# Optimization experiments

Hardware: AMD Instinct MI355X
Metric: run time of the kernel (lower is better)

## Reference

```python
import jax, jax.numpy as jnp
import numpy as np

BNK, L, DIN, DOUT, NREL = 1280, 64, 512, 256, 40

def setup_inputs() -> dict:
    key = jax.random.key(0)
    ks = jax.random.split(key, 10)
    rep = jax.random.normal(ks[0], (BNK, L, DIN), dtype=jnp.float32)
    # adj_arc_in[..., 0] = flattened sentence index, adj_arc_in[..., 1] = head token position
    sent = jnp.broadcast_to(jnp.arange(BNK, dtype=jnp.int64)[:, None], (BNK, L))
    head = jax.random.randint(ks[1], (BNK, L), 0, L, dtype=jnp.int64)
    adj_arc_in = jnp.stack([sent, head], axis=-1)  # [BNK, L, 2]
    adj_lab_in = jax.random.randint(ks[2], (BNK, L), 0, NREL, dtype=jnp.int64)
    adj_mask_in = (jax.random.uniform(ks[3], (BNK, L)) < 0.9).astype(jnp.float32)
    adj_mask_loop = jnp.ones((BNK, L), dtype=jnp.float32)
    mask = jnp.ones((BNK, L), dtype=jnp.float32)
    # parameters (xavier-ish init)
    W_in = jax.random.normal(ks[4], (DIN, DOUT), dtype=jnp.float32) * (2.0 / (DIN + DOUT)) ** 0.5
    b_in = jnp.zeros((NREL, DOUT), dtype=jnp.float32)
    W_gate_in = jax.random.uniform(ks[5], (DIN, 1), dtype=jnp.float32)
    b_gate_in = jnp.ones((NREL, 1), dtype=jnp.float32)
    W_self = jax.random.normal(ks[6], (DIN, DOUT), dtype=jnp.float32) * (2.0 / (DIN + DOUT)) ** 0.5
    W_gate_self = jax.random.uniform(ks[7], (DIN, 1), dtype=jnp.float32)
    return {"rep": rep, "adj_mask_in": adj_mask_in, "adj_mask_loop": adj_mask_loop,
            "mask": mask, "W_in": W_in, "b_in": b_in, "W_gate_in": W_gate_in,
            "b_gate_in": b_gate_in, "W_self": W_self, "W_gate_self": W_gate_self,
            "adj_arc_in": adj_arc_in, "adj_lab_in": adj_lab_in}

def reference(rep, adj_mask_in, adj_mask_loop, mask, W_in, b_in, W_gate_in,
              b_gate_in, W_self, W_gate_self, adj_arc_in, adj_lab_in):
    bnk, l, din = rep.shape
    dout = W_in.shape[1]
    rep_ = rep.reshape(bnk * l, din)                    # [M, Din]
    idx = adj_arc_in[..., 0].reshape(-1) * l + adj_arc_in[..., 1].reshape(-1)  # [M]
    lab = adj_lab_in.reshape(-1)                        # [M]
    # in-arc potential: gather projected head token, add relation-typed bias
    in_pot = (rep_ @ W_in)[idx] + b_in[lab]             # [M, Dout]
    in_gate = (rep_ @ W_gate_in)[idx, 0] + b_gate_in[lab, 0]  # [M]
    # self-loop potential
    self_pot = rep_ @ W_self                            # [M, Dout]
    self_gate = (rep_ @ W_gate_self)[:, 0]              # [M]
    pots = jnp.stack([in_pot, self_pot], axis=1)        # [M, 2, Dout]
    gates = jnp.stack([in_gate, self_gate], axis=1)     # [M, 2]
    msoft = jnp.stack([adj_mask_in.reshape(-1), adj_mask_loop.reshape(-1)], axis=1)  # [M, 2]
    # original multiplies by mask_soft twice: potentials * mask_soft * (sigmoid(gate) * mask_soft)
    w = jax.nn.sigmoid(gates) * msoft * msoft           # [M, 2]
    res = jax.nn.relu(jnp.einsum('mdk,md->mk', pots, w))  # [M, Dout]
    res = res.reshape(bnk, l, dout) * mask.reshape(bnk, l)[..., None]
    return res
```

## Files before the change

kernel.cpp:

```cpp
#include <hip/hip_runtime.h>


#define BNKS  1280
#define LTOK  64
#define DIN   512
#define DOUT  256
#define TPB   256

typedef __attribute__((ext_vector_type(4))) float f32x4;
typedef __attribute__((ext_vector_type(2))) float f32x2;
typedef __attribute__((ext_vector_type(8))) short s16x8;

__device__ __forceinline__ unsigned pack_bf16(float a, float b) {
  const unsigned ua = __float_as_uint(a), ub = __float_as_uint(b);
  return ((ua + 0x8000u) >> 16) | ((ub + 0x8000u) & 0xffff0000u);
}
__device__ __forceinline__ unsigned short f2bf(float f) {
  return (unsigned short)((__float_as_uint(f) + 0x8000u) >> 16);
}
__device__ __forceinline__ float bf2f(unsigned short h) {
  return __uint_as_float(((unsigned)h) << 16);
}
__device__ __forceinline__ float sigm(float x) { return 1.0f / (1.0f + __expf(-x)); }
__device__ __forceinline__ float dot4(f32x4 a, f32x4 b) {
  return a.x * b.x + a.y * b.y + a.z * b.z + a.w * b.w;
}
__device__ __forceinline__ s16x8 pack8(f32x4 a, f32x4 b) {
  union { uint4 u; s16x8 v; } r;
  r.u.x = pack_bf16(a.x, a.y); r.u.y = pack_bf16(a.z, a.w);
  r.u.z = pack_bf16(b.x, b.y); r.u.w = pack_bf16(b.z, b.w);
  return r.v;
}

__global__ __launch_bounds__(256) void wprep_kernel(const float* __restrict__ W_in,
                                                    const float* __restrict__ W_self,
                                                    unsigned short* __restrict__ Wt) {
  __shared__ float tile[32][33];
  const int t  = threadIdx.x;
  const int c0 = (blockIdx.x & 15) * 32;
  const int k0 = (blockIdx.x >> 4) * 32;
  const float* src = (c0 < DOUT) ? W_in : W_self;
  const int cadj   = (c0 < DOUT) ? c0 : (c0 - DOUT);
  {
    const int kk = t >> 3;
    const int cc = (t & 7) * 4;
    const float4 v = *(const float4*)(src + (size_t)(k0 + kk) * DOUT + cadj + cc);
    tile[kk][cc + 0] = v.x; tile[kk][cc + 1] = v.y;
    tile[kk][cc + 2] = v.z; tile[kk][cc + 3] = v.w;
  }
  __syncthreads();
  {
    const int cc = t >> 3;
    const int kk = (t & 7) * 4;
    ushort4 o;
    o.x = f2bf(tile[kk + 0][cc]); o.y = f2bf(tile[kk + 1][cc]);
    o.z = f2bf(tile[kk + 2][cc]); o.w = f2bf(tile[kk + 3][cc]);
    *(ushort4*)(Wt + (size_t)(c0 + cc) * DIN + k0 + kk) = o;
  }
}

__global__ __launch_bounds__(TPB, 2) void gcn_kernel(
    const float* __restrict__ rep,
    const float* __restrict__ adj_mask_in,
    const float* __restrict__ maskp,
    const float* __restrict__ b_in,
    const float* __restrict__ w_gate_in,
    const float* __restrict__ b_gate_in,
    const float* __restrict__ w_gate_self,
    const int* __restrict__ arc,
    const int* __restrict__ lab,
    const unsigned short* __restrict__ Wt,
    float* __restrict__ out)
{
  __shared__ __align__(16) char smem[46080];
  float* wgiL = (float*)smem;
  float* wgsL = (float*)(smem + 2048);

  const int t    = threadIdx.x;
  const int wave = t >> 6;
  const int lane = t & 63;
  const int nlo  = lane & 15;
  const int quad = lane >> 4;

  char* wbase = smem + 4096 + wave * 10496;
  unsigned short* PinW = (unsigned short*)wbase;
  float* winW = (float*)(wbase + 8704);
  float* wslW = (float*)(wbase + 8960);
  float* mskW = (float*)(wbase + 9216);
  int*   hdW  = (int*)  (wbase + 9472);
  int*   lbW  = (int*)  (wbase + 9728);
  float* giW  = (float*)(wbase + 9984);
  float* gsW  = (float*)(wbase + 10240);

  const int bid = blockIdx.x;
  const int cg  = bid & 3;
  const int sq  = bid >> 2;
  const int s   = sq * 4 + wave;
  const int n0  = cg * 64;

  *(f32x2*)(wgiL + 2 * t) = *(const f32x2*)(w_gate_in  + 2 * t);
  *(f32x2*)(wgsL + 2 * t) = *(const f32x2*)(w_gate_self + 2 * t);
  __syncthreads();

  const float* arow = rep + ((size_t)s * LTOK + nlo) * DIN;
  const unsigned short* wq = Wt + (size_t)nlo * DIN + quad * 8;

  f32x4 acc[4][8];
  #pragma unroll
  for (int i = 0; i < 4; ++i)
    #pragma unroll
    for (int j = 0; j < 8; ++j) { f32x4 z = {0.f,0.f,0.f,0.f}; acc[i][j] = z; }
  float gip[4] = {0.f,0.f,0.f,0.f}, gsp[4] = {0.f,0.f,0.f,0.f};

  f32x4 Ar[4][2];
  #pragma unroll
  for (int mt = 0; mt < 4; ++mt) {
    const float* p = arow + (size_t)(mt * 16) * DIN + quad * 8;
    Ar[mt][0] = *(const f32x4*)p;
    Ar[mt][1] = *(const f32x4*)(p + 4);
  }

  for (int kc = 0; kc < 16; ++kc) {
    const int ko = kc * 32 + quad * 8;

    s16x8 Bc[8];
    #pragma unroll
    for (int nt = 0; nt < 8; ++nt) {
      const int catbase = (nt < 4) ? (n0 + nt * 16) : (DOUT + n0 + (nt - 4) * 16);
      Bc[nt] = *(const s16x8*)(wq + (size_t)catbase * DIN + kc * 32);
    }

    const f32x4 wi0 = *(const f32x4*)(wgiL + ko);
    const f32x4 wi1 = *(const f32x4*)(wgiL + ko + 4);
    const f32x4 ws0 = *(const f32x4*)(wgsL + ko);
    const f32x4 ws1 = *(const f32x4*)(wgsL + ko + 4);
    s16x8 af[4];
    #pragma unroll
    for (int mt = 0; mt < 4; ++mt) {
      const f32x4 a0 = Ar[mt][0], a1 = Ar[mt][1];
      gip[mt] += dot4(a0, wi0) + dot4(a1, wi1);
      gsp[mt] += dot4(a0, ws0) + dot4(a1, ws1);
      af[mt] = pack8(a0, a1);
    }

    if (kc < 15) {
      #pragma unroll
      for (int mt = 0; mt < 4; ++mt) {
        const float* p = arow + (size_t)(mt * 16) * DIN + (kc + 1) * 32 + quad * 8;
        Ar[mt][0] = *(const f32x4*)p;
        Ar[mt][1] = *(const f32x4*)(p + 4);
      }
    }

    #pragma unroll
    for (int nt = 0; nt < 8; ++nt)
      #pragma unroll
      for (int mt = 0; mt < 4; ++mt)
        acc[mt][nt] = __builtin_amdgcn_mfma_f32_16x16x32_bf16(af[mt], Bc[nt], acc[mt][nt], 0, 0, 0);
  }

  #pragma unroll
  for (int mt = 0; mt < 4; ++mt) {
    gip[mt] += __shfl_xor(gip[mt], 16, 64);
    gip[mt] += __shfl_xor(gip[mt], 32, 64);
    gsp[mt] += __shfl_xor(gsp[mt], 16, 64);
    gsp[mt] += __shfl_xor(gsp[mt], 32, 64);
  }
  if (quad == 0) {
    #pragma unroll
    for (int mt = 0; mt < 4; ++mt) {
      giW[mt * 16 + nlo] = gip[mt];
      gsW[mt * 16 + nlo] = gsp[mt];
    }
  }
  #pragma unroll
  for (int mt = 0; mt < 4; ++mt)
    #pragma unroll
    for (int nt = 0; nt < 4; ++nt)
      #pragma unroll
      for (int rr = 0; rr < 4; ++rr)
        PinW[(mt * 16 + quad * 4 + rr) * 68 + nt * 16 + nlo] = f2bf(acc[mt][nt][rr]);
  __syncthreads();

  {
    const int m  = s * LTOK + lane;
    const int hd = arc[2 * m + 1];
    const int lb = lab[m];
    const float am = adj_mask_in[m];
    hdW[lane] = hd;
    lbW[lane] = lb;
    mskW[lane] = maskp[m];
    winW[lane] = sigm(giW[hd] + b_gate_in[lb]) * am * am;
    wslW[lane] = sigm(gsW[lane]);
  }
  __syncthreads();

  #pragma unroll
  for (int mt = 0; mt < 4; ++mt) {
    const int rb = mt * 16 + quad * 4;
    const f32x4 wi4 = *(const f32x4*)(winW + rb);
    const f32x4 ws4 = *(const f32x4*)(wslW + rb);
    const f32x4 mk4 = *(const f32x4*)(mskW + rb);
    union { int4 v; int a[4]; } hd4, lb4;
    hd4.v = *(const int4*)(hdW + rb);
    lb4.v = *(const int4*)(lbW + rb);
    #pragma unroll
    for (int rr = 0; rr < 4; ++rr) {
      const float wi = wi4[rr], ws = ws4[rr], mk = mk4[rr];
      const int hd = hd4.a[rr], lb = lb4.a[rr];
      float* orow = out + (size_t)(s * LTOK + rb + rr) * DOUT + n0;
      #pragma unroll
      for (int nt = 0; nt < 4; ++nt) {
        const int col = nt * 16 + nlo;
        const float pin = bf2f(PinW[hd * 68 + col]);
        const float bi  = b_in[(size_t)lb * DOUT + n0 + col];
        const float o   = (pin + bi) * wi + acc[mt][nt + 4][rr] * ws;
        orow[col] = fmaxf(o, 0.f) * mk;
      }
    }
  }
}

extern "C" void kernel_launch(void* const* d_in, const int* in_sizes, int n_in,
                              void* d_out, int out_size, void* d_ws, size_t ws_size,
                              hipStream_t stream) {
  const float* rep           = (const float*)d_in[0];
  const float* adj_mask_in   = (const float*)d_in[1];
  const float* mask          = (const float*)d_in[3];
  const float* W_in          = (const float*)d_in[4];
  const float* b_in          = (const float*)d_in[5];
  const float* W_gate_in     = (const float*)d_in[6];
  const float* b_gate_in     = (const float*)d_in[7];
  const float* W_self        = (const float*)d_in[8];
  const float* W_gate_self   = (const float*)d_in[9];
  const int*   arc           = (const int*)d_in[10];
  const int*   lab           = (const int*)d_in[11];
  float* out = (float*)d_out;
  unsigned short* Wt = (unsigned short*)d_ws;

  wprep_kernel<<<256, 256, 0, stream>>>(W_in, W_self, Wt);
  gcn_kernel<<<BNKS, TPB, 0, stream>>>(rep, adj_mask_in, mask, b_in,
                                       W_gate_in, b_gate_in, W_gate_self,
                                       arc, lab, Wt, out);
}
```

Before: 411.7 us.

## Share sentence A tile across 8 waves via double-buffered swizzled LDS

Each block now handles one whole sentence with 512 threads, and each wave owns a 32-column slice of both W_in and W_self. Before, four column-group blocks each reloaded the full rep rows for a sentence. The rep tile is now loaded once cooperatively, converted to bf16 and staged into a double-buffered, XOR-swizzled LDS buffer that all waves read. Gate dot products are split across threads and reduced through LDS. The change removes the 4x redundant rep reads and fp32-to-bf16 conversions, and cuts accumulator registers so more waves can be resident. The cost is a block-wide barrier on every k-step and higher per-element W loads per wave.

```diff
diff --git a/kernel.cpp b/kernel.cpp
--- a/kernel.cpp
+++ b/kernel.cpp
@@ -5,10 +5,11 @@
 #define LTOK  64
 #define DIN   512
 #define DOUT  256
-#define TPB   256
+#define TPB   512
+
+#define LDS_TOTAL 42752
 
 typedef __attribute__((ext_vector_type(4))) float f32x4;
-typedef __attribute__((ext_vector_type(2))) float f32x2;
 typedef __attribute__((ext_vector_type(8))) short s16x8;
 
 __device__ __forceinline__ unsigned pack_bf16(float a, float b) {
@@ -24,12 +25,6 @@
 __device__ __forceinline__ float sigm(float x) { return 1.0f / (1.0f + __expf(-x)); }
 __device__ __forceinline__ float dot4(f32x4 a, f32x4 b) {
   return a.x * b.x + a.y * b.y + a.z * b.z + a.w * b.w;
-}
-__device__ __forceinline__ s16x8 pack8(f32x4 a, f32x4 b) {
-  union { uint4 u; s16x8 v; } r;
-  r.u.x = pack_bf16(a.x, a.y); r.u.y = pack_bf16(a.z, a.w);
-  r.u.z = pack_bf16(b.x, b.y); r.u.w = pack_bf16(b.z, b.w);
-  return r.v;
 }
 
 __global__ __launch_bounds__(256) void wprep_kernel(const float* __restrict__ W_in,
@@ -59,7 +54,11 @@
   }
 }
 
-__global__ __launch_bounds__(TPB, 2) void gcn_kernel(
+__device__ __forceinline__ int apos(int row, int u) {
+  return u ^ (row & 3) ^ ((row >> 2) & 3);
+}
+
+__global__ __launch_bounds__(TPB, 4) void gcn_kernel(
     const float* __restrict__ rep,
     const float* __restrict__ adj_mask_in,
     const float* __restrict__ maskp,
@@ -72,150 +71,147 @@
     const unsigned short* __restrict__ Wt,
     float* __restrict__ out)
 {
-  __shared__ __align__(16) char smem[46080];
-  float* wgiL = (float*)smem;
-  float* wgsL = (float*)(smem + 2048);
-
+  __shared__ __align__(16) char smem[LDS_TOTAL];
+  float* wgiL = (float*)(smem + 8192);
+  float* wgsL = (float*)(smem + 10240);
+  float* gpL  = (float*)(smem + 36864);
+  float* giA  = (float*)(smem + 40960);
+  float* wslA = (float*)(smem + 40960 + 256);
+  float* winA = (float*)(smem + 40960 + 512);
+  float* amA  = (float*)(smem + 40960 + 768);
+  float* mskA = (float*)(smem + 40960 + 1024);
+  int*   hdA  = (int*)  (smem + 40960 + 1280);
+  int*   lbA  = (int*)  (smem + 40960 + 1536);
+
+  const int s    = blockIdx.x;
   const int t    = threadIdx.x;
   const int wave = t >> 6;
   const int lane = t & 63;
   const int nlo  = lane & 15;
   const int quad = lane >> 4;
 
-  char* wbase = smem + 4096 + wave * 10496;
-  unsigned short* PinW = (unsigned short*)wbase;
-  float* winW = (float*)(wbase + 8704);
-  float* wslW = (float*)(wbase + 8960);
-  float* mskW = (float*)(wbase + 9216);
-  int*   hdW  = (int*)  (wbase + 9472);
-  int*   lbW  = (int*)  (wbase + 9728);
-  float* giW  = (float*)(wbase + 9984);
-  float* gsW  = (float*)(wbase + 10240);
-
-  const int bid = blockIdx.x;
-  const int cg  = bid & 3;
-  const int sq  = bid >> 2;
-  const int s   = sq * 4 + wave;
-  const int n0  = cg * 64;
-
-  *(f32x2*)(wgiL + 2 * t) = *(const f32x2*)(w_gate_in  + 2 * t);
-  *(f32x2*)(wgsL + 2 * t) = *(const f32x2*)(w_gate_self + 2 * t);
-  __syncthreads();
-
-  const float* arow = rep + ((size_t)s * LTOK + nlo) * DIN;
-  const unsigned short* wq = Wt + (size_t)nlo * DIN + quad * 8;
-
-  f32x4 acc[4][8];
+  unsigned short* PinW = (unsigned short*)(smem) + wave * 2304;
+
+  const int srow = t >> 3;
+  const int skq  = t & 7;
+  char* const awr = smem + srow * 64 + apos(srow, skq >> 1) * 16 + (skq & 1) * 8;
+  const float* const arep = rep + ((size_t)s * LTOK + srow) * DIN + skq * 4;
+
+  if (t < 128) {
+    *(f32x4*)(wgiL + 4 * t) = *(const f32x4*)(w_gate_in   + 4 * t);
+    *(f32x4*)(wgsL + 4 * t) = *(const f32x4*)(w_gate_self + 4 * t);
+  }
+
+  f32x4 acc[4][4];
   #pragma unroll
   for (int i = 0; i < 4; ++i)
     #pragma unroll
-    for (int j = 0; j < 8; ++j) { f32x4 z = {0.f,0.f,0.f,0.f}; acc[i][j] = z; }
-  float gip[4] = {0.f,0.f,0.f,0.f}, gsp[4] = {0.f,0.f,0.f,0.f};
-
-  f32x4 Ar[4][2];
+    for (int j = 0; j < 4; ++j) { f32x4 z = {0.f,0.f,0.f,0.f}; acc[i][j] = z; }
+  float gi = 0.f, gs = 0.f;
+
+  const unsigned short* const wqi = Wt + ((size_t)(wave * 32) + nlo) * DIN + quad * 8;
+
+  __syncthreads();
+
+  {
+    const f32x4 a = *(const f32x4*)(arep);
+    gi += dot4(a, *(const f32x4*)(wgiL + skq * 4));
+    gs += dot4(a, *(const f32x4*)(wgsL + skq * 4));
+    unsigned* w2 = (unsigned*)awr;
+    w2[0] = pack_bf16(a.x, a.y);
+    w2[1] = pack_bf16(a.z, a.w);
+  }
+  __syncthreads();
+
+  for (int kc = 0; kc < 16; ++kc) {
+    const int p = kc & 1;
+    char* const buf = smem + p * 4096;
+
+    s16x8 af[4];
+    #pragma unroll
+    for (int mt = 0; mt < 4; ++mt) {
+      const int row = mt * 16 + nlo;
+      af[mt] = *(const s16x8*)(buf + row * 64 + apos(row, quad) * 16);
+    }
+
+    s16x8 Bc[4];
+    #pragma unroll
+    for (int j = 0; j < 4; ++j) {
+      const size_t cofs = (j < 2) ? ((size_t)(j * 16) * DIN)
+                                  : ((size_t)(DOUT + (j - 2) * 16) * DIN);
+      Bc[j] = *(const s16x8*)(wqi + cofs + kc * 32);
+    }
+
+    if (kc < 15) {
+      const f32x4 a = *(const f32x4*)(arep + (kc + 1) * 32);
+      const int ko = (kc + 1) * 32 + skq * 4;
+      gi += dot4(a, *(const f32x4*)(wgiL + ko));
+      gs += dot4(a, *(const f32x4*)(wgsL + ko));
+      unsigned* w2 = (unsigned*)(awr + (p ^ 1) * 4096);
+      w2[0] = pack_bf16(a.x, a.y);
+      w2[1] = pack_bf16(a.z, a.w);
+    }
+    __syncthreads();
+
+    #pragma unroll
+    for (int j = 0; j < 4; ++j)
+      #pragma unroll
+      for (int mt = 0; mt < 4; ++mt)
+        acc[mt][j] = __builtin_amdgcn_mfma_f32_16x16x32_bf16(af[mt], Bc[j], acc[mt][j], 0, 0, 0);
+  }
+
+  gpL[srow * 16 + skq * 2 + 0] = gi;
+  gpL[srow * 16 + skq * 2 + 1] = gs;
+
+  #pragma unroll
+  for (int mt = 0; mt < 4; ++mt)
+    #pragma unroll
+    for (int j = 0; j < 2; ++j)
+      #pragma unroll
+      for (int r = 0; r < 4; ++r) {
+        const int row = mt * 16 + quad * 4 + r;
+        PinW[row * 36 + j * 16 + nlo] = f2bf(acc[mt][j][r]);
+      }
+  __syncthreads();
+
+  if (t < LTOK) {
+    float g0 = 0.f, g1 = 0.f;
+    #pragma unroll
+    for (int q = 0; q < 8; ++q) {
+      g0 += gpL[t * 16 + q * 2 + 0];
+      g1 += gpL[t * 16 + q * 2 + 1];
+    }
+    const int m = s * LTOK + t;
+    giA[t]  = g0;
+    wslA[t] = sigm(g1);
+    amA[t]  = adj_mask_in[m];
+    mskA[t] = maskp[m];
+    hdA[t]  = arc[2 * m + 1];
+    lbA[t]  = lab[m];
+  }
+  __syncthreads();
+  if (t < LTOK) {
+    const float am = amA[t];
+    winA[t] = sigm(giA[hdA[t]] + b_gate_in[lbA[t]]) * am * am;
+  }
+  __syncthreads();
+
+  const int n0w = wave * 32;
   #pragma unroll
   for (int mt = 0; mt < 4; ++mt) {
-    const float* p = arow + (size_t)(mt * 16) * DIN + quad * 8;
-    Ar[mt][0] = *(const f32x4*)p;
-    Ar[mt][1] = *(const f32x4*)(p + 4);
-  }
-
-  for (int kc = 0; kc < 16; ++kc) {
-    const int ko = kc * 32 + quad * 8;
-
-    s16x8 Bc[8];
-    #pragma unroll
-    for (int nt = 0; nt < 8; ++nt) {
-      const int catbase = (nt < 4) ? (n0 + nt * 16) : (DOUT + n0 + (nt - 4) * 16);
-      Bc[nt] = *(const s16x8*)(wq + (size_t)catbase * DIN + kc * 32);
-    }
-
-    const f32x4 wi0 = *(const f32x4*)(wgiL + ko);
-    const f32x4 wi1 = *(const f32x4*)(wgiL + ko + 4);
-    const f32x4 ws0 = *(const f32x4*)(wgsL + ko);
-    const f32x4 ws1 = *(const f32x4*)(wgsL + ko + 4);
-    s16x8 af[4];
-    #pragma unroll
-    for (int mt = 0; mt < 4; ++mt) {
-      const f32x4 a0 = Ar[mt][0], a1 = Ar[mt][1];
-      gip[mt] += dot4(a0, wi0) + dot4(a1, wi1);
-      gsp[mt] += dot4(a0, ws0) + dot4(a1, ws1);
-      af[mt] = pack8(a0, a1);
-    }
-
-    if (kc < 15) {
+    #pragma unroll
+    for (int r = 0; r < 4; ++r) {
+      const int row = mt * 16 + quad * 4 + r;
+      const float wi = winA[row], ws = wslA[row], mk = mskA[row];
+      const int hd = hdA[row], lb = lbA[row];
+      float* orow = out + ((size_t)s * LTOK + row) * DOUT + n0w;
+      const float* birow = b_in + (size_t)lb * DOUT + n0w;
       #pragma unroll
-      for (int mt = 0; mt < 4; ++mt) {
-        const float* p = arow + (size_t)(mt * 16) * DIN + (kc + 1) * 32 + quad * 8;
-        Ar[mt][0] = *(const f32x4*)p;
-        Ar[mt][1] = *(const f32x4*)(p + 4);
-      }
-    }
-
-    #pragma unroll
-    for (int nt = 0; nt < 8; ++nt)
-      #pragma unroll
-      for (int mt = 0; mt < 4; ++mt)
-        acc[mt][nt] = __builtin_amdgcn_mfma_f32_16x16x32_bf16(af[mt], Bc[nt], acc[mt][nt], 0, 0, 0);
-  }
-
-  #pragma unroll
-  for (int mt = 0; mt < 4; ++mt) {
-    gip[mt] += __shfl_xor(gip[mt], 16, 64);
-    gip[mt] += __shfl_xor(gip[mt], 32, 64);
-    gsp[mt] += __shfl_xor(gsp[mt], 16, 64);
-    gsp[mt] += __shfl_xor(gsp[mt], 32, 64);
-  }
-  if (quad == 0) {
-    #pragma unroll
-    for (int mt = 0; mt < 4; ++mt) {
-      giW[mt * 16 + nlo] = gip[mt];
-      gsW[mt * 16 + nlo] = gsp[mt];
-    }
-  }
-  #pragma unroll
-  for (int mt = 0; mt < 4; ++mt)
-    #pragma unroll
-    for (int nt = 0; nt < 4; ++nt)
-      #pragma unroll
-      for (int rr = 0; rr < 4; ++rr)
-        PinW[(mt * 16 + quad * 4 + rr) * 68 + nt * 16 + nlo] = f2bf(acc[mt][nt][rr]);
-  __syncthreads();
-
-  {
-    const int m  = s * LTOK + lane;
-    const int hd = arc[2 * m + 1];
-    const int lb = lab[m];
-    const float am = adj_mask_in[m];
-    hdW[lane] = hd;
-    lbW[lane] = lb;
-    mskW[lane] = maskp[m];
-    winW[lane] = sigm(giW[hd] + b_gate_in[lb]) * am * am;
-    wslW[lane] = sigm(gsW[lane]);
-  }
-  __syncthreads();
-
-  #pragma unroll
-  for (int mt = 0; mt < 4; ++mt) {
-    const int rb = mt * 16 + quad * 4;
-    const f32x4 wi4 = *(const f32x4*)(winW + rb);
-    const f32x4 ws4 = *(const f32x4*)(wslW + rb);
-    const f32x4 mk4 = *(const f32x4*)(mskW + rb);
-    union { int4 v; int a[4]; } hd4, lb4;
-    hd4.v = *(const int4*)(hdW + rb);
-    lb4.v = *(const int4*)(lbW + rb);
-    #pragma unroll
-    for (int rr = 0; rr < 4; ++rr) {
-      const float wi = wi4[rr], ws = ws4[rr], mk = mk4[rr];
-      const int hd = hd4.a[rr], lb = lb4.a[rr];
-      float* orow = out + (size_t)(s * LTOK + rb + rr) * DOUT + n0;
-      #pragma unroll
-      for (int nt = 0; nt < 4; ++nt) {
-        const int col = nt * 16 + nlo;
-        const float pin = bf2f(PinW[hd * 68 + col]);
-        const float bi  = b_in[(size_t)lb * DOUT + n0 + col];
-        const float o   = (pin + bi) * wi + acc[mt][nt + 4][rr] * ws;
-        orow[col] = fmaxf(o, 0.f) * mk;
+      for (int j = 0; j < 2; ++j) {
+        const int c = j * 16 + nlo;
+        const float pin = bf2f(PinW[hd * 36 + c]);
+        const float o = (pin + birow[c]) * wi + acc[mt][j + 2][r] * ws;
+        orow[c] = fmaxf(o, 0.f) * mk;
       }
     }
   }
```

Result: slower. 588.8 us (+43.0%).
